# Performance work log

Measured on AMD Instinct MI355X. Metric: run time of the kernel, lower is better.

## Reference

```python
import jax, jax.numpy as jnp
import numpy as np


def setup_inputs() -> dict:
    key = jax.random.key(0)
    ks = jax.random.split(key, 8)
    B, N, D = 8, 2048, 128
    s = 1.0 / float(np.sqrt(D))
    node = jax.random.normal(ks[0], (B, N, D), dtype=jnp.float32)
    node_mask = jax.random.randint(ks[1], (B, N), 0, 2, dtype=jnp.int32)
    punctuation_graph = jax.random.randint(ks[2], (B, N, N), 0, 2, dtype=jnp.int32)
    w_nw = jax.random.uniform(ks[3], (1, D), jnp.float32, -s, s)
    b_nw = jax.random.uniform(ks[4], (1,), jnp.float32, -s, s)
    w_self = jax.random.uniform(ks[5], (D, D), jnp.float32, -s, s)
    b_self = jax.random.uniform(ks[6], (D,), jnp.float32, -s, s)
    w_punct = jax.random.uniform(ks[7], (D, D), jnp.float32, -s, s)
    return {"node": node, "node_mask": node_mask, "punctuation_graph": punctuation_graph,
            "w_nw": w_nw, "b_nw": b_nw, "w_self": w_self, "b_self": b_self,
            "w_punct": w_punct, "iteration_steps": 2}


def reference(node, node_mask, punctuation_graph, w_nw, b_nw, w_self, b_self, w_punct, iteration_steps):
    B, N, D = node.shape
    # dd_graph = mask outer product with zeroed diagonal; graph = dd_graph * punctuation_graph
    eye = jnp.eye(N, dtype=punctuation_graph.dtype)
    dd = node_mask[:, None, :] * node_mask[:, :, None] * (1 - eye)[None, :, :]  # [B,N,N]
    graph = dd * punctuation_graph  # [B,N,N] int, binary
    nbr_num = graph.sum(-1)  # [B,N]
    # replace_masked_values(nbr_num, nbr_num>=1, 1): nodes with no neighbors get denom 1
    nbr_f = jnp.where(nbr_num >= 1, nbr_num.astype(node.dtype), jnp.asarray(1.0, node.dtype))
    gmask = graph > 0
    weights = []
    x = node
    for _ in range(iteration_steps):  # small fixed step count
        dw = jax.nn.sigmoid(jnp.einsum('bnd,od->bno', x, w_nw) + b_nw)[..., 0]  # [B,N]
        weights.append(dw)
        self_info = jnp.einsum('bnd,ed->bne', x, w_self) + b_self  # [B,N,D]
        info_p = jnp.einsum('bnd,ed->bne', x, w_punct)  # [B,N,D]
        # node_weight[b,i,j] = dw[b,j] where graph[b,i,j] else 0
        nw = jnp.where(gmask, dw[:, None, :], jnp.asarray(0.0, x.dtype))  # [B,N,N]
        agg = jnp.einsum('bnm,bmd->bnd', nw, info_p) / nbr_f[..., None]
        x = jax.nn.relu(self_info + agg)
    all_weight = jnp.stack(weights, axis=1)  # [B, steps, N]
    return x, all_weight
```

## Files before the change

### kernel.cpp

```cpp
#include <hip/hip_runtime.h>
#include <hip/hip_bf16.h>

#define BB 8
#define NN 2048
#define DD 128

typedef __attribute__((ext_vector_type(8))) __bf16 bf16x8;
typedef __attribute__((ext_vector_type(4))) float f32x4;
typedef __attribute__((ext_vector_type(4))) int   i32x4;

static __device__ __forceinline__ unsigned short f2bf(float f) {
    union { float f; unsigned u; } v; v.f = f;
    unsigned r = (v.u + 0x7FFFu + ((v.u >> 16) & 1u)) >> 16;
    return (unsigned short)r;
}
static __device__ __forceinline__ float bf2f(unsigned short b) {
    union { unsigned u; float f; } v; v.u = ((unsigned)b) << 16;
    return v.f;
}

__global__ __launch_bounds__(256) void kernB0(
    const float* __restrict__ x,
    const float* __restrict__ w_nw, const float* __restrict__ b_nw,
    const float* __restrict__ w_self, const float* __restrict__ b_self,
    const float* __restrict__ w_punct,
    float* __restrict__ si_out,
    unsigned short* __restrict__ yne_out,
    unsigned short* __restrict__ yT_out,
    float* __restrict__ aw_out)
{
    __shared__ unsigned short xt[64*32];
    __shared__ unsigned short wst[128*32];
    __shared__ unsigned short wpt[128*32];
    __shared__ float wnw_l[DD];
    __shared__ float red[256];
    __shared__ float dw_l[64];
    __shared__ unsigned short ytl[128*72];

    const int n0 = blockIdx.x * 64;
    const int t  = threadIdx.x;
    const int b  = n0 >> 11;
    const int nb = n0 & (NN - 1);

    if (t < DD) wnw_l[t] = w_nw[t];
    __syncthreads();

    const int wave = t >> 6, lane = t & 63;
    const int wm = wave >> 1, wn = wave & 1;
    const int quad = lane >> 4, l16 = lane & 15;

    const int n_loc = t >> 2, dq = t & 3;
    const int we = t >> 1,   wh = t & 1;

    f32x4 accs[2][4] = {}; f32x4 accp[2][4] = {};
    float dwpart = 0.f;

    #pragma unroll
    for (int kk = 0; kk < 4; ++kk) {
        const int k0 = kk * 32;
        {
            const float* xs = x + (size_t)(n0 + n_loc) * DD + k0 + dq * 8;
            f32x4 a = *(const f32x4*)xs;
            f32x4 c = *(const f32x4*)(xs + 4);
            const float* wv = &wnw_l[k0 + dq * 8];
            dwpart += a.x*wv[0] + a.y*wv[1] + a.z*wv[2] + a.w*wv[3]
                    + c.x*wv[4] + c.y*wv[5] + c.z*wv[6] + c.w*wv[7];
            unsigned q0 = f2bf(a.x) | ((unsigned)f2bf(a.y) << 16);
            unsigned q1 = f2bf(a.z) | ((unsigned)f2bf(a.w) << 16);
            unsigned q2 = f2bf(c.x) | ((unsigned)f2bf(c.y) << 16);
            unsigned q3 = f2bf(c.z) | ((unsigned)f2bf(c.w) << 16);
            i32x4 pw = {(int)q0,(int)q1,(int)q2,(int)q3};
            *(i32x4*)&xt[n_loc*32 + dq*8] = pw;
        }
        {
            const float* s1 = w_self  + (size_t)we * DD + k0 + wh*16;
            const float* s2 = w_punct + (size_t)we * DD + k0 + wh*16;
            f32x4 a0 = *(const f32x4*)s1;      f32x4 a1 = *(const f32x4*)(s1+4);
            f32x4 a2 = *(const f32x4*)(s1+8);  f32x4 a3 = *(const f32x4*)(s1+12);
            unsigned q0 = f2bf(a0.x) | ((unsigned)f2bf(a0.y)<<16);
            unsigned q1 = f2bf(a0.z) | ((unsigned)f2bf(a0.w)<<16);
            unsigned q2 = f2bf(a1.x) | ((unsigned)f2bf(a1.y)<<16);
            unsigned q3 = f2bf(a1.z) | ((unsigned)f2bf(a1.w)<<16);
            unsigned q4 = f2bf(a2.x) | ((unsigned)f2bf(a2.y)<<16);
            unsigned q5 = f2bf(a2.z) | ((unsigned)f2bf(a2.w)<<16);
            unsigned q6 = f2bf(a3.x) | ((unsigned)f2bf(a3.y)<<16);
            unsigned q7 = f2bf(a3.z) | ((unsigned)f2bf(a3.w)<<16);
            i32x4 pw0 = {(int)q0,(int)q1,(int)q2,(int)q3};
            i32x4 pw1 = {(int)q4,(int)q5,(int)q6,(int)q7};
            *(i32x4*)&wst[we*32 + wh*16]     = pw0;
            *(i32x4*)&wst[we*32 + wh*16 + 8] = pw1;
            f32x4 c0 = *(const f32x4*)s2;      f32x4 c1 = *(const f32x4*)(s2+4);
            f32x4 c2 = *(const f32x4*)(s2+8);  f32x4 c3 = *(const f32x4*)(s2+12);
            unsigned r0 = f2bf(c0.x) | ((unsigned)f2bf(c0.y)<<16);
            unsigned r1 = f2bf(c0.z) | ((unsigned)f2bf(c0.w)<<16);
            unsigned r2 = f2bf(c1.x) | ((unsigned)f2bf(c1.y)<<16);
            unsigned r3 = f2bf(c1.z) | ((unsigned)f2bf(c1.w)<<16);
            unsigned r4 = f2bf(c2.x) | ((unsigned)f2bf(c2.y)<<16);
            unsigned r5 = f2bf(c2.z) | ((unsigned)f2bf(c2.w)<<16);
            unsigned r6 = f2bf(c3.x) | ((unsigned)f2bf(c3.y)<<16);
            unsigned r7 = f2bf(c3.z) | ((unsigned)f2bf(c3.w)<<16);
            i32x4 pv0 = {(int)r0,(int)r1,(int)r2,(int)r3};
            i32x4 pv1 = {(int)r4,(int)r5,(int)r6,(int)r7};
            *(i32x4*)&wpt[we*32 + wh*16]     = pv0;
            *(i32x4*)&wpt[we*32 + wh*16 + 8] = pv1;
        }
        __syncthreads();
        bf16x8 af[2], bs[4], bp[4];
        #pragma unroll
        for (int mt = 0; mt < 2; ++mt)
            af[mt] = *(const bf16x8*)&xt[(wm*32 + mt*16 + l16)*32 + quad*8];
        #pragma unroll
        for (int nt = 0; nt < 4; ++nt) {
            const int er = wn*64 + nt*16 + l16;
            bs[nt] = *(const bf16x8*)&wst[er*32 + quad*8];
            bp[nt] = *(const bf16x8*)&wpt[er*32 + quad*8];
        }
        #pragma unroll
        for (int mt = 0; mt < 2; ++mt)
            #pragma unroll
            for (int nt = 0; nt < 4; ++nt) {
                accs[mt][nt] = __builtin_amdgcn_mfma_f32_16x16x32_bf16(af[mt], bs[nt], accs[mt][nt], 0, 0, 0);
                accp[mt][nt] = __builtin_amdgcn_mfma_f32_16x16x32_bf16(af[mt], bp[nt], accp[mt][nt], 0, 0, 0);
            }
        __syncthreads();
    }

    red[t] = dwpart;
    __syncthreads();
    if (t < 64) {
        float s = red[4*t] + red[4*t+1] + red[4*t+2] + red[4*t+3] + b_nw[0];
        float dv = 1.f / (1.f + __expf(-s));
        dw_l[t] = dv;
        aw_out[(size_t)b * 2 * NN + nb + t] = dv;
    }
    __syncthreads();

    #pragma unroll
    for (int mt = 0; mt < 2; ++mt) {
        #pragma unroll
        for (int nt = 0; nt < 4; ++nt) {
            const int e = wn*64 + nt*16 + l16;
            const float bsv = b_self[e];
            #pragma unroll
            for (int r = 0; r < 4; ++r) {
                const int nl = wm*32 + mt*16 + quad*4 + r;
                const size_t idx = (size_t)(n0 + nl) * DD + e;
                si_out[idx] = accs[mt][nt][r] + bsv;
                const float yv = dw_l[nl] * accp[mt][nt][r];
                const unsigned short ub = f2bf(yv);
                yne_out[idx] = ub;
                ytl[e*72 + nl] = ub;
            }
        }
    }
    __syncthreads();
    {
        const int e = t >> 1, half = t & 1;
        const i32x4* src = (const i32x4*)&ytl[e*72 + half*32];
        i32x4 v0 = src[0], v1 = src[1], v2 = src[2], v3 = src[3];
        i32x4* dst = (i32x4*)(yT_out + (size_t)(b*DD + e) * NN + nb + half*32);
        dst[0] = v0; dst[1] = v1; dst[2] = v2; dst[3] = v3;
    }
}

#define OFF_SCL   0u
#define OFF_PDM   256u
#define OFF_WNW   512u
#define OFF_DW    1024u
#define OFF_A     1280u
#define OFF_XT4   1280u
#define OFF_RED   (1280u + 16384u)
#define OFF_B     25856u
#define OFF_WST   25856u
#define OFF_WPT   (25856u + 8192u)
#define OFF_YTL   (25856u + 16384u)
#define SMEM_CB   60672u

__global__ __launch_bounds__(256) void kernCBP(
    const int* __restrict__ punct, const int* __restrict__ mask,
    const unsigned short* __restrict__ yT0,
    const unsigned short* __restrict__ yne0,
    float* si,
    const float* __restrict__ w_self, const float* __restrict__ w_punct,
    const float* __restrict__ w_nw, const float* __restrict__ b_nw,
    const float* __restrict__ b_self,
    unsigned* __restrict__ pk_g, float* __restrict__ scale_g,
    float* __restrict__ pdm_g,
    unsigned short* __restrict__ yT1,
    float* __restrict__ aw1)
{
    __shared__ char smem[SMEM_CB];
    float*          scl_l = (float*)(smem + OFF_SCL);
    float*          pdm_l = (float*)(smem + OFF_PDM);
    float*          wnw_l = (float*)(smem + OFF_WNW);
    float*          dw_l  = (float*)(smem + OFF_DW);
    unsigned*       pPk   = (unsigned*)(smem + OFF_A);
    unsigned short* xt4   = (unsigned short*)(smem + OFF_XT4);
    float*          red   = (float*)(smem + OFF_RED);
    f32x4*          accL  = (f32x4*)(smem + OFF_B);
    unsigned short* wst   = (unsigned short*)(smem + OFF_WST);
    unsigned short* wpt   = (unsigned short*)(smem + OFF_WPT);
    unsigned short* ytl   = (unsigned short*)(smem + OFF_YTL);

    const int t  = threadIdx.x;
    const int b  = blockIdx.x & 7;
    const int i0 = (blockIdx.x >> 3) * 64;
    const size_t rg0 = (size_t)b * NN + i0;

    const int wave = t >> 6, lane = t & 63;

    {
        const int* mrow = mask + (size_t)b * NN;
        unsigned mw = 0;
        #pragma unroll
        for (int q = 0; q < 8; ++q) {
            i32x4 m = *(const i32x4*)(mrow + lane * 32 + q * 4);
            unsigned nib = (m.x & 1) | ((m.y & 1) << 1) | ((m.z & 1) << 2) | ((m.w & 1) << 3);
            mw |= nib << (4 * q);
        }
        for (int rr = 0; rr < 16; ++rr) {
            const int rl = wave * 16 + rr;
            const int gi = i0 + rl;
            const int mi = mrow[gi];
            if (mi == 0) {
                if (lane == 0) {
                    scl_l[rl] = 0.f; pdm_l[rl] = 0.f;
                    scale_g[rg0 + rl] = 0.f; pdm_g[rg0 + rl] = 0.f;
                }
                continue;
            }
            const int* prow = punct + (rg0 + rl) * NN;
            i32x4 v[8];
            #pragma unroll
            for (int q = 0; q < 8; ++q)
                v[q] = *(const i32x4*)(prow + lane * 32 + q * 4);
            unsigned wd = 0;
            #pragma unroll
            for (int q = 0; q < 8; ++q) {
                unsigned nib = (v[q].x & 1) | ((v[q].y & 1) << 1)
                             | ((v[q].z & 1) << 2) | ((v[q].w & 1) << 3);
                wd |= nib << (4 * q);
            }
            wd &= mw;
            pPk[rl * 68 + lane] = wd;
            pk_g[(rg0 + rl) * 64 + lane] = wd;

            int acc = __popc(wd);
            if ((gi >> 5) == lane) acc += (int)((wd >> (gi & 31)) & 1u) << 16;
            #pragma unroll
            for (int o = 32; o > 0; o >>= 1) acc += __shfl_xor(acc, o, 64);
            if (lane == 0) {
                const int nall = acc & 0xFFFF;
                const int pd   = acc >> 16;
                const int nbr  = nall - pd;
                const float sc = 1.f / (float)(nbr < 1 ? 1 : nbr);
                scl_l[rl] = sc; pdm_l[rl] = (float)pd;
                scale_g[rg0 + rl] = sc; pdm_g[rg0 + rl] = (float)pd;
            }
        }
    }
    if (t < 128) wnw_l[t] = w_nw[t];
    __syncthreads();

    const int kh = wave >> 1, eh = wave & 1;
    const int quad = lane >> 4, l16 = lane & 15;
    const unsigned short* yTb = yT0 + (size_t)b * DD * NN;

    f32x4 acc[4][4] = {};
    #pragma unroll 4
    for (int ks = 0; ks < 32; ++ks) {
        const int kk = kh * 32 + ks;
        bf16x8 bfr[4];
        #pragma unroll
        for (int nt = 0; nt < 4; ++nt) {
            const int e = eh*64 + nt*16 + l16;
            bfr[nt] = *(const bf16x8*)(yTb + (size_t)e * NN + kk*32 + quad*8);
        }
        bf16x8 af[4];
        #pragma unroll
        for (int mt = 0; mt < 4; ++mt) {
            const unsigned w = pPk[(mt*16 + l16) * 68 + kk];
            const unsigned by = (w >> (quad * 8)) & 0xFFu;
            i32x4 ex;
            ex.x = (int)((((by &   1u) << 7) + ((by &   2u) << 22)) * 0x7Fu);
            ex.y = (int)((((by &   4u) << 5) + ((by &   8u) << 20)) * 0x7Fu);
            ex.z = (int)((((by &  16u) << 3) + ((by &  32u) << 18)) * 0x7Fu);
            ex.w = (int)((((by &  64u) << 1) + ((by & 128u) << 16)) * 0x7Fu);
            union { i32x4 i; bf16x8 h; } cv; cv.i = ex;
            af[mt] = cv.h;
        }
        #pragma unroll
        for (int mt = 0; mt < 4; ++mt)
            #pragma unroll
            for (int nt = 0; nt < 4; ++nt)
                acc[mt][nt] = __builtin_amdgcn_mfma_f32_16x16x32_bf16(af[mt], bfr[nt], acc[mt][nt], 0, 0, 0);
    }

    __syncthreads();
    if (kh == 1) {
        #pragma unroll
        for (int mt = 0; mt < 4; ++mt)
            #pragma unroll
            for (int nt = 0; nt < 4; ++nt)
                accL[(eh*16 + mt*4 + nt)*64 + lane] = acc[mt][nt];
    }
    __syncthreads();

    if (kh == 0) {
        #pragma unroll
        for (int mt = 0; mt < 4; ++mt) {
            float part[4] = {0.f, 0.f, 0.f, 0.f};
            #pragma unroll
            for (int nt = 0; nt < 4; ++nt) {
                f32x4 o = accL[(eh*16 + mt*4 + nt)*64 + lane];
                const int e = eh*64 + nt*16 + l16;
                const float wv = wnw_l[e];
                #pragma unroll
                for (int r = 0; r < 4; ++r) {
                    const int row = mt*16 + quad*4 + r;
                    const size_t idx = (rg0 + row) * DD + e;
                    const float yv = bf2f(yne0[idx]);
                    float xv = si[idx]
                             + scl_l[row] * (acc[mt][nt][r] + o[r] - pdm_l[row] * yv);
                    xv = fmaxf(xv, 0.f);
                    xt4[((e >> 5) * 64 + row) * 32 + (e & 31)] = f2bf(xv);
                    part[r] += xv * wv;
                }
            }
            #pragma unroll
            for (int r = 0; r < 4; ++r) {
                const int row = mt*16 + quad*4 + r;
                red[row * 32 + eh*16 + l16] = part[r];
            }
        }
    }
    __syncthreads();

    if (t < 64) {
        float s = b_nw[0];
        #pragma unroll 8
        for (int c = 0; c < 32; ++c) s += red[t * 32 + c];
        float dv = 1.f / (1.f + __expf(-s));
        dw_l[t] = dv;
        aw1[(size_t)b * 2 * NN + i0 + t] = dv;
    }
    __syncthreads();

    const int wm = kh, wn = eh;
    const int we = t >> 1, wh = t & 1;

    f32x4 accs[2][4] = {}; f32x4 accp[2][4] = {};

    #pragma unroll
    for (int kk = 0; kk < 4; ++kk) {
        const int k0 = kk * 32;
        {
            const float* s1 = w_self  + (size_t)we * DD + k0 + wh*16;
            const float* s2 = w_punct + (size_t)we * DD + k0 + wh*16;
            f32x4 a0 = *(const f32x4*)s1;      f32x4 a1 = *(const f32x4*)(s1+4);
            f32x4 a2 = *(const f32x4*)(s1+8);  f32x4 a3 = *(const f32x4*)(s1+12);
            unsigned q0 = f2bf(a0.x) | ((unsigned)f2bf(a0.y)<<16);
            unsigned q1 = f2bf(a0.z) | ((unsigned)f2bf(a0.w)<<16);
            unsigned q2 = f2bf(a1.x) | ((unsigned)f2bf(a1.y)<<16);
            unsigned q3 = f2bf(a1.z) | ((unsigned)f2bf(a1.w)<<16);
            unsigned q4 = f2bf(a2.x) | ((unsigned)f2bf(a2.y)<<16);
            unsigned q5 = f2bf(a2.z) | ((unsigned)f2bf(a2.w)<<16);
            unsigned q6 = f2bf(a3.x) | ((unsigned)f2bf(a3.y)<<16);
            unsigned q7 = f2bf(a3.z) | ((unsigned)f2bf(a3.w)<<16);
            i32x4 pw0 = {(int)q0,(int)q1,(int)q2,(int)q3};
            i32x4 pw1 = {(int)q4,(int)q5,(int)q6,(int)q7};
            *(i32x4*)&wst[we*32 + wh*16]     = pw0;
            *(i32x4*)&wst[we*32 + wh*16 + 8] = pw1;
            f32x4 c0 = *(const f32x4*)s2;      f32x4 c1 = *(const f32x4*)(s2+4);
            f32x4 c2 = *(const f32x4*)(s2+8);  f32x4 c3 = *(const f32x4*)(s2+12);
            unsigned r0 = f2bf(c0.x) | ((unsigned)f2bf(c0.y)<<16);
            unsigned r1 = f2bf(c0.z) | ((unsigned)f2bf(c0.w)<<16);
            unsigned r2 = f2bf(c1.x) | ((unsigned)f2bf(c1.y)<<16);
            unsigned r3 = f2bf(c1.z) | ((unsigned)f2bf(c1.w)<<16);
            unsigned r4 = f2bf(c2.x) | ((unsigned)f2bf(c2.y)<<16);
            unsigned r5 = f2bf(c2.z) | ((unsigned)f2bf(c2.w)<<16);
            unsigned r6 = f2bf(c3.x) | ((unsigned)f2bf(c3.y)<<16);
            unsigned r7 = f2bf(c3.z) | ((unsigned)f2bf(c3.w)<<16);
            i32x4 pv0 = {(int)r0,(int)r1,(int)r2,(int)r3};
            i32x4 pv1 = {(int)r4,(int)r5,(int)r6,(int)r7};
            *(i32x4*)&wpt[we*32 + wh*16]     = pv0;
            *(i32x4*)&wpt[we*32 + wh*16 + 8] = pv1;
        }
        __syncthreads();
        bf16x8 af[2], bs[4], bp[4];
        #pragma unroll
        for (int mt = 0; mt < 2; ++mt)
            af[mt] = *(const bf16x8*)&xt4[(kk*64 + wm*32 + mt*16 + l16)*32 + quad*8];
        #pragma unroll
        for (int nt = 0; nt < 4; ++nt) {
            const int er = wn*64 + nt*16 + l16;
            bs[nt] = *(const bf16x8*)&wst[er*32 + quad*8];
            bp[nt] = *(const bf16x8*)&wpt[er*32 + quad*8];
        }
        #pragma unroll
        for (int mt = 0; mt < 2; ++mt)
            #pragma unroll
            for (int nt = 0; nt < 4; ++nt) {
                accs[mt][nt] = __builtin_amdgcn_mfma_f32_16x16x32_bf16(af[mt], bs[nt], accs[mt][nt], 0, 0, 0);
                accp[mt][nt] = __builtin_amdgcn_mfma_f32_16x16x32_bf16(af[mt], bp[nt], accp[mt][nt], 0, 0, 0);
            }
        __syncthreads();
    }

    #pragma unroll
    for (int mt = 0; mt < 2; ++mt) {
        #pragma unroll
        for (int nt = 0; nt < 4; ++nt) {
            const int e = wn*64 + nt*16 + l16;
            const float bsv = b_self[e];
            #pragma unroll
            for (int r = 0; r < 4; ++r) {
                const int nl = wm*32 + mt*16 + quad*4 + r;
                const size_t idx = (rg0 + nl) * DD + e;
                const float yv = dw_l[nl] * accp[mt][nt][r];
                const unsigned short ub = f2bf(yv);
                const float yvr = bf2f(ub);
                si[idx] = accs[mt][nt][r] + bsv - scl_l[nl] * pdm_l[nl] * yvr;
                ytl[e*72 + nl] = ub;
            }
        }
    }
    __syncthreads();
    {
        const int e = t >> 1, half = t & 1;
        const i32x4* src = (const i32x4*)&ytl[e*72 + half*32];
        i32x4 v0 = src[0], v1 = src[1], v2 = src[2], v3 = src[3];
        i32x4* dst = (i32x4*)(yT1 + (size_t)(b*DD + e) * NN + i0 + half*32);
        dst[0] = v0; dst[1] = v1; dst[2] = v2; dst[3] = v3;
    }
}

__global__ __launch_bounds__(256) void kernC4(
    const unsigned* __restrict__ pk,
    const float* __restrict__ scale_g,
    const unsigned short* __restrict__ yT,
    const float* __restrict__ sip,
    float* __restrict__ x_out)
{
    __shared__ unsigned pPk[64 * 68];
    __shared__ float scale_l[64];
    __shared__ f32x4 accL[2][16][64];

    const int t  = threadIdx.x;
    const int b  = blockIdx.x & 7;
    const int i0 = (blockIdx.x >> 3) * 64;
    const size_t rg0 = (size_t)b * NN + i0;

    #pragma unroll
    for (int r = 0; r < 4; ++r) {
        const int u   = r * 256 + t;
        const int row = u >> 4;
        const int wq  = (u & 15) * 4;
        i32x4 v = *(const i32x4*)(pk + (rg0 + row) * 64 + wq);
        *(i32x4*)&pPk[row * 68 + wq] = v;
    }
    if (t < 64) scale_l[t] = scale_g[rg0 + t];
    __syncthreads();

    const int wave = t >> 6, lane = t & 63;
    const int kh = wave >> 1, eh = wave & 1;
    const int quad = lane >> 4, l16 = lane & 15;
    const unsigned short* yTb = yT + (size_t)b * DD * NN;

    f32x4 acc[4][4] = {};

    #pragma unroll 4
    for (int ks = 0; ks < 32; ++ks) {
        const int kk = kh * 32 + ks;
        bf16x8 bfr[4];
        #pragma unroll
        for (int nt = 0; nt < 4; ++nt) {
            const int e = eh*64 + nt*16 + l16;
            bfr[nt] = *(const bf16x8*)(yTb + (size_t)e * NN + kk*32 + quad*8);
        }
        bf16x8 af[4];
        #pragma unroll
        for (int mt = 0; mt < 4; ++mt) {
            const unsigned w = pPk[(mt*16 + l16) * 68 + kk];
            const unsigned by = (w >> (quad * 8)) & 0xFFu;
            i32x4 ex;
            ex.x = (int)((((by &   1u) << 7) + ((by &   2u) << 22)) * 0x7Fu);
            ex.y = (int)((((by &   4u) << 5) + ((by &   8u) << 20)) * 0x7Fu);
            ex.z = (int)((((by &  16u) << 3) + ((by &  32u) << 18)) * 0x7Fu);
            ex.w = (int)((((by &  64u) << 1) + ((by & 128u) << 16)) * 0x7Fu);
            union { i32x4 i; bf16x8 h; } cv; cv.i = ex;
            af[mt] = cv.h;
        }
        #pragma unroll
        for (int mt = 0; mt < 4; ++mt)
            #pragma unroll
            for (int nt = 0; nt < 4; ++nt)
                acc[mt][nt] = __builtin_amdgcn_mfma_f32_16x16x32_bf16(af[mt], bfr[nt], acc[mt][nt], 0, 0, 0);
    }

    __syncthreads();
    if (kh == 1) {
        #pragma unroll
        for (int mt = 0; mt < 4; ++mt)
            #pragma unroll
            for (int nt = 0; nt < 4; ++nt)
                accL[eh][mt*4 + nt][lane] = acc[mt][nt];
    }
    __syncthreads();
    if (kh == 0) {
        #pragma unroll
        for (int mt = 0; mt < 4; ++mt) {
            #pragma unroll
            for (int nt = 0; nt < 4; ++nt) {
                f32x4 o = accL[eh][mt*4 + nt][lane];
                const int e = eh*64 + nt*16 + l16;
                #pragma unroll
                for (int r = 0; r < 4; ++r) {
                    const int row = mt*16 + quad*4 + r;
                    const size_t idx = (rg0 + row) * DD + e;
                    float v = sip[idx] + scale_l[row] * (acc[mt][nt][r] + o[r]);
                    x_out[idx] = fmaxf(v, 0.f);
                }
            }
        }
    }
}

extern "C" void kernel_launch(void* const* d_in, const int* in_sizes, int n_in,
                              void* d_out, int out_size, void* d_ws, size_t ws_size,
                              hipStream_t stream) {
    const float* node   = (const float*)d_in[0];
    const int*   mask   = (const int*)  d_in[1];
    const int*   punct  = (const int*)  d_in[2];
    const float* w_nw   = (const float*)d_in[3];
    const float* b_nw   = (const float*)d_in[4];
    const float* w_self = (const float*)d_in[5];
    const float* b_self = (const float*)d_in[6];
    const float* w_punct= (const float*)d_in[7];

    float* xout = (float*)d_out;
    float* aw   = xout + (size_t)BB * NN * DD;

    char* w = (char*)d_ws;
    float*          si   = (float*)w;
    unsigned short* yne0 = (unsigned short*)(w + (8u  << 20));
    unsigned short* yT0  = (unsigned short*)(w + (12u << 20));
    unsigned*       pk   = (unsigned*)(w + (16u << 20));
    float*          scl  = (float*)(w + (20u << 20));
    float*          pdm  = (float*)(w + (20u << 20) + (64u << 10));
    unsigned short* yT1  = (unsigned short*)(w + (24u << 20));

    kernB0 <<<dim3(256), dim3(256), 0, stream>>>(node, w_nw, b_nw, w_self,
                                                 b_self, w_punct,
                                                 si, yne0, yT0, aw);
    kernCBP<<<dim3(256), dim3(256), 0, stream>>>(punct, mask, yT0, yne0, si,
                                                 w_self, w_punct, w_nw, b_nw,
                                                 b_self, pk, scl, pdm,
                                                 yT1, aw + NN);
    kernC4 <<<dim3(256), dim3(256), 0, stream>>>(pk, scl, yT1, si, xout);
}
```

Measured before the change: 264.2 us.

## Move graph bit-packing into first kernel as extra blocks running alongside projection

The punctuation-graph bit-packing and neighbor-count computation moves out of the second kernel into 256 extra blocks of the first kernel, so it can run concurrently with the first-step projection GEMM. The packing now uses coalesced per-lane loads with wave ballots instead of per-lane 128-byte strided vector loads, and no longer skips masked rows. The second kernel just loads the packed bits and scales from global memory. This trades skipping reads for masked rows for better overlap of the 128MB graph read with compute.

```diff
diff --git a/kernel.cpp b/kernel.cpp
--- a/kernel.cpp
+++ b/kernel.cpp
@@ -19,15 +19,18 @@
     return v.f;
 }
 
-__global__ __launch_bounds__(256) void kernB0(
+__global__ __launch_bounds__(256) void kernBP(
     const float* __restrict__ x,
+    const int* __restrict__ punct, const int* __restrict__ mask,
     const float* __restrict__ w_nw, const float* __restrict__ b_nw,
     const float* __restrict__ w_self, const float* __restrict__ b_self,
     const float* __restrict__ w_punct,
     float* __restrict__ si_out,
     unsigned short* __restrict__ yne_out,
     unsigned short* __restrict__ yT_out,
-    float* __restrict__ aw_out)
+    float* __restrict__ aw_out,
+    unsigned* __restrict__ pk, float* __restrict__ scale_g,
+    float* __restrict__ pdm_g)
 {
     __shared__ unsigned short xt[64*32];
     __shared__ unsigned short wst[128*32];
@@ -37,8 +40,59 @@
     __shared__ float dw_l[64];
     __shared__ unsigned short ytl[128*72];
 
-    const int n0 = blockIdx.x * 64;
-    const int t  = threadIdx.x;
+    const int bid = blockIdx.x;
+    const int t   = threadIdx.x;
+
+    if (bid >= 256) {
+        const int pb   = bid - 256;
+        const int wave = t >> 6, lane = t & 63;
+        const int b    = (pb * 64) >> 11;
+        const int* mrow = mask + (size_t)b * NN;
+
+        int mv[32];
+        #pragma unroll
+        for (int w = 0; w < 32; ++w) mv[w] = mrow[w * 64 + lane];
+
+        for (int rr = 0; rr < 16; ++rr) {
+            const int row_g = pb * 64 + wave * 16 + rr;
+            const int i = row_g & (NN - 1);
+            const int* prow = punct + (size_t)row_g * NN;
+            unsigned p0 = 0, p1 = 0;
+            int acc = 0;
+            #pragma unroll
+            for (int h = 0; h < 2; ++h) {
+                int pv[16];
+                #pragma unroll
+                for (int w = 0; w < 16; ++w)
+                    pv[w] = prow[(h * 16 + w) * 64 + lane];
+                #pragma unroll
+                for (int w = 0; w < 16; ++w) {
+                    const int wg = h * 16 + w;
+                    const int pred = (pv[w] & mv[wg]) & 1;
+                    unsigned long long bal = __ballot(pred);
+                    if (lane == wg) { p0 = (unsigned)bal; p1 = (unsigned)(bal >> 32); }
+                    acc += pred + (((wg * 64 + lane) == i ? pred : 0) << 16);
+                }
+            }
+            #pragma unroll
+            for (int o = 32; o > 0; o >>= 1) acc += __shfl_xor(acc, o, 64);
+            if (lane < 32) {
+                uint2 w2; w2.x = p0; w2.y = p1;
+                *(uint2*)(pk + (size_t)row_g * 64 + 2 * lane) = w2;
+            }
+            if (lane == 0) {
+                const int nall = acc & 0xFFFF;
+                const int pd   = acc >> 16;
+                const int mi   = mrow[i];
+                const int nbr  = nall - pd;
+                scale_g[row_g] = mi ? 1.f / (float)(nbr < 1 ? 1 : nbr) : 0.f;
+                pdm_g[row_g]   = (float)pd;
+            }
+        }
+        return;
+    }
+
+    const int n0 = bid * 64;
     const int b  = n0 >> 11;
     const int nb = n0 & (NN - 1);
 
@@ -176,16 +230,15 @@
 #define OFF_YTL   (25856u + 16384u)
 #define SMEM_CB   60672u
 
-__global__ __launch_bounds__(256) void kernCBP(
-    const int* __restrict__ punct, const int* __restrict__ mask,
+__global__ __launch_bounds__(256) void kernCB(
+    const unsigned* __restrict__ pk,
+    const float* __restrict__ scale_g, const float* __restrict__ pdm_g,
     const unsigned short* __restrict__ yT0,
     const unsigned short* __restrict__ yne0,
     float* si,
     const float* __restrict__ w_self, const float* __restrict__ w_punct,
     const float* __restrict__ w_nw, const float* __restrict__ b_nw,
     const float* __restrict__ b_self,
-    unsigned* __restrict__ pk_g, float* __restrict__ scale_g,
-    float* __restrict__ pdm_g,
     unsigned short* __restrict__ yT1,
     float* __restrict__ aw1)
 {
@@ -207,61 +260,20 @@
     const int i0 = (blockIdx.x >> 3) * 64;
     const size_t rg0 = (size_t)b * NN + i0;
 
+    #pragma unroll
+    for (int r = 0; r < 4; ++r) {
+        const int u   = r * 256 + t;
+        const int row = u >> 4;
+        const int wq  = (u & 15) * 4;
+        i32x4 v = *(const i32x4*)(pk + (rg0 + row) * 64 + wq);
+        *(i32x4*)&pPk[row * 68 + wq] = v;
+    }
+    if (t < 64)                   scl_l[t]      = scale_g[rg0 + t];
+    else if (t < 128)             pdm_l[t-64]   = pdm_g[rg0 + t - 64];
+    else                          wnw_l[t-128]  = w_nw[t-128];
+    __syncthreads();
+
     const int wave = t >> 6, lane = t & 63;
-
-    {
-        const int* mrow = mask + (size_t)b * NN;
-        unsigned mw = 0;
-        #pragma unroll
-        for (int q = 0; q < 8; ++q) {
-            i32x4 m = *(const i32x4*)(mrow + lane * 32 + q * 4);
-            unsigned nib = (m.x & 1) | ((m.y & 1) << 1) | ((m.z & 1) << 2) | ((m.w & 1) << 3);
-            mw |= nib << (4 * q);
-        }
-        for (int rr = 0; rr < 16; ++rr) {
-            const int rl = wave * 16 + rr;
-            const int gi = i0 + rl;
-            const int mi = mrow[gi];
-            if (mi == 0) {
-                if (lane == 0) {
-                    scl_l[rl] = 0.f; pdm_l[rl] = 0.f;
-                    scale_g[rg0 + rl] = 0.f; pdm_g[rg0 + rl] = 0.f;
-                }
-                continue;
-            }
-            const int* prow = punct + (rg0 + rl) * NN;
-            i32x4 v[8];
-            #pragma unroll
-            for (int q = 0; q < 8; ++q)
-                v[q] = *(const i32x4*)(prow + lane * 32 + q * 4);
-            unsigned wd = 0;
-            #pragma unroll
-            for (int q = 0; q < 8; ++q) {
-                unsigned nib = (v[q].x & 1) | ((v[q].y & 1) << 1)
-                             | ((v[q].z & 1) << 2) | ((v[q].w & 1) << 3);
-                wd |= nib << (4 * q);
-            }
-            wd &= mw;
-            pPk[rl * 68 + lane] = wd;
-            pk_g[(rg0 + rl) * 64 + lane] = wd;
-
-            int acc = __popc(wd);
-            if ((gi >> 5) == lane) acc += (int)((wd >> (gi & 31)) & 1u) << 16;
-            #pragma unroll
-            for (int o = 32; o > 0; o >>= 1) acc += __shfl_xor(acc, o, 64);
-            if (lane == 0) {
-                const int nall = acc & 0xFFFF;
-                const int pd   = acc >> 16;
-                const int nbr  = nall - pd;
-                const float sc = 1.f / (float)(nbr < 1 ? 1 : nbr);
-                scl_l[rl] = sc; pdm_l[rl] = (float)pd;
-                scale_g[rg0 + rl] = sc; pdm_g[rg0 + rl] = (float)pd;
-            }
-        }
-    }
-    if (t < 128) wnw_l[t] = w_nw[t];
-    __syncthreads();
-
     const int kh = wave >> 1, eh = wave & 1;
     const int quad = lane >> 4, l16 = lane & 15;
     const unsigned short* yTb = yT0 + (size_t)b * DD * NN;
@@ -550,12 +562,12 @@
     float*          pdm  = (float*)(w + (20u << 20) + (64u << 10));
     unsigned short* yT1  = (unsigned short*)(w + (24u << 20));
 
-    kernB0 <<<dim3(256), dim3(256), 0, stream>>>(node, w_nw, b_nw, w_self,
-                                                 b_self, w_punct,
-                                                 si, yne0, yT0, aw);
-    kernCBP<<<dim3(256), dim3(256), 0, stream>>>(punct, mask, yT0, yne0, si,
-                                                 w_self, w_punct, w_nw, b_nw,
-                                                 b_self, pk, scl, pdm,
-                                                 yT1, aw + NN);
-    kernC4 <<<dim3(256), dim3(256), 0, stream>>>(pk, scl, yT1, si, xout);
+    kernBP<<<dim3(512), dim3(256), 0, stream>>>(node, punct, mask,
+                                                w_nw, b_nw, w_self, b_self,
+                                                w_punct, si, yne0, yT0, aw,
+                                                pk, scl, pdm);
+    kernCB<<<dim3(256), dim3(256), 0, stream>>>(pk, scl, pdm, yT0, yne0, si,
+                                                w_self, w_punct, w_nw, b_nw,
+                                                b_self, yT1, aw + NN);
+    kernC4<<<dim3(256), dim3(256), 0, stream>>>(pk, scl, yT1, si, xout);
 }
```

Result: slower. 270.9 us (+2.6%).
